# Kernel tuning notes

Measured on AMD Instinct MI355X. Metric: run time of the kernel, lower is better.

## Reference

```python
import jax, jax.numpy as jnp
import numpy as np

N_NODES = 100000
N_EDGES = 3200000
F_IN, H_ENC, H_GCN, H_Q, A_DIM = 128, 128, 128, 256, 10


def setup_inputs() -> dict:
    key = jax.random.key(0)
    ks = jax.random.split(key, 8)
    s = lambda d: 1.0 / np.sqrt(d)
    return {
        "x": jax.random.normal(ks[0], (N_NODES, F_IN), jnp.float32),
        "edge_index": jax.random.randint(ks[1], (2, N_EDGES), 0, N_NODES, jnp.int64),
        "W_enc": jax.random.normal(ks[2], (F_IN, H_ENC), jnp.float32) * s(F_IN),
        "b_enc": jnp.zeros((H_ENC,), jnp.float32),
        "W_gcn": jax.random.normal(ks[3], (H_ENC, H_GCN), jnp.float32) * s(H_ENC),
        "b_gcn": jnp.zeros((H_GCN,), jnp.float32),
        "W1": jax.random.normal(ks[4], (H_GCN, H_Q), jnp.float32) * s(H_GCN),
        "b1": jnp.zeros((H_Q,), jnp.float32),
        "W2": jax.random.normal(ks[5], (H_Q, A_DIM), jnp.float32) * s(H_Q),
        "b2": jnp.zeros((A_DIM,), jnp.float32),
    }


def gcn_conv(x, edge_index, W, b):
    # Standard GCNConv: D^{-1/2} (A + I) D^{-1/2} X W + b, symmetric norm with self-loops.
    n = x.shape[0]
    src, dst = edge_index[0], edge_index[1]
    xw = x @ W  # [N, H]
    deg = jnp.ones((n,), xw.dtype).at[dst].add(1.0)  # in-degree + self-loop
    dinv = jax.lax.rsqrt(deg)
    coef = dinv[src] * dinv[dst]  # [E]
    msg = xw[src] * coef[:, None]  # [E, H] gather-scale
    agg = jax.ops.segment_sum(msg, dst, num_segments=n)  # scatter-add
    agg = agg + xw * (dinv * dinv)[:, None]  # self-loop contribution
    return agg + b


def reference(x, edge_index, W_enc, b_enc, W_gcn, b_gcn, W1, b1, W2, b2):
    h = jax.nn.relu(x @ W_enc + b_enc)              # Encoder: Linear + ReLU
    h = jax.nn.relu(gcn_conv(h, edge_index, W_gcn, b_gcn))  # GCNConv + ReLU
    q = jax.nn.relu(h @ W1 + b1) @ W2 + b2          # Q_Net MLP
    return q
```

## Files before the change

### kernel.cpp

```cpp
#include <hip/hip_runtime.h>

#define N_NODES 100000
constexpr int F     = 128;
constexpr int NB    = (N_NODES + 63) / 64;
constexpr int BCAP  = 2560;
constexpr int LCAP  = 80;
constexpr int CHUNK = 8192;
constexpr int PADN  = N_NODES;

typedef __attribute__((ext_vector_type(8))) short short8;
typedef __attribute__((ext_vector_type(4))) float f32x4;
typedef __attribute__((ext_vector_type(4))) short short4v;
typedef __attribute__((ext_vector_type(4))) unsigned uint4v;

__device__ inline short f2bf(float v) {
    union { float f; unsigned u; } x; x.f = v;
    unsigned r = (x.u + 0x7fff + ((x.u >> 16) & 1)) >> 16;
    return (short)r;
}
__device__ inline float lo_bf(unsigned v) {
    union { unsigned u; float f; } x; x.u = v << 16; return x.f;
}
__device__ inline float hi_bf(unsigned v) {
    union { unsigned u; float f; } x; x.u = v & 0xffff0000u; return x.f;
}

__global__ __launch_bounds__(256) void prep_kernel(const float* __restrict__ W_enc,
                                                   const float* __restrict__ W_gcn,
                                                   const float* __restrict__ W1,
                                                   const float* __restrict__ W2,
                                                   short* __restrict__ Wte,
                                                   short* __restrict__ Wtg,
                                                   short* __restrict__ Wt1,
                                                   short* __restrict__ W2t,
                                                   int* __restrict__ bcr) {
    int idx = blockIdx.x * 256 + threadIdx.x;
    if (idx < 16384) { int h = idx >> 7, k = idx & 127; Wte[idx] = f2bf(W_enc[k * 128 + h]); return; }
    idx -= 16384;
    if (idx < 16384) { int h = idx >> 7, k = idx & 127; Wtg[idx] = f2bf(W_gcn[k * 128 + h]); return; }
    idx -= 16384;
    if (idx < 32768) { int h = idx >> 7, k = idx & 127; Wt1[idx] = f2bf(W1[k * 256 + h]); return; }
    idx -= 32768;
    if (idx < 4096)  { int n = idx >> 8, k = idx & 255; W2t[idx] = (n < 10) ? f2bf(W2[k * 10 + n]) : (short)0; return; }
    idx -= 4096;
    if (idx < NB) bcr[idx] = 0;
}

__global__ __launch_bounds__(512) void part_kernel(const int* __restrict__ src,
                                                   const int* __restrict__ dst,
                                                   int* __restrict__ bcur,
                                                   int* __restrict__ part, int E) {
    __shared__ int cnt[NB];
    __shared__ int base[NB];
    for (int b = threadIdx.x; b < NB; b += 512) cnt[b] = 0;
    __syncthreads();
    const int e0 = blockIdx.x * CHUNK;
    const int e1 = min(e0 + CHUNK, E);
#pragma unroll 4
    for (int e = e0 + threadIdx.x; e < e1; e += 512)
        atomicAdd(&cnt[dst[e] >> 6], 1);
    __syncthreads();
    for (int b = threadIdx.x; b < NB; b += 512) {
        int c = cnt[b];
        base[b] = c ? atomicAdd(&bcur[b], c) : 0;
        cnt[b] = 0;
    }
    __syncthreads();
#pragma unroll 4
    for (int e = e0 + threadIdx.x; e < e1; e += 512) {
        int d = dst[e];
        int b = d >> 6;
        int idx = base[b] + atomicAdd(&cnt[b], 1);
        if (idx < BCAP) part[b * BCAP + idx] = src[e] | ((d & 63) << 17);
    }
}

__global__ __launch_bounds__(256) void gemmA_kernel(const float* __restrict__ x,
                                                    const short* __restrict__ Wte,
                                                    const short* __restrict__ Wtg,
                                                    const float* __restrict__ b_enc,
                                                    const int* __restrict__ bcur,
                                                    const int* __restrict__ part,
                                                    short* __restrict__ xs) {
    __shared__ int deg_l[64];
    __shared__ short h_l[4][16][136];
    const int b = blockIdx.x;
    if (threadIdx.x < 64) deg_l[threadIdx.x] = 0;
    __syncthreads();
    const int cnt = min(bcur[b], BCAP);
    const int* p = part + (size_t)b * BCAP;
#pragma unroll 4
    for (int i = threadIdx.x; i < cnt; i += 256)
        atomicAdd(&deg_l[(p[i] >> 17) & 63], 1);

    const int wave = threadIdx.x >> 6;
    const int lane = threadIdx.x & 63;
    const int quad = lane >> 4;
    const int l16  = lane & 15;
    const int node0 = b * 64 + wave * 16;
    int nrow = node0 + l16;
    const bool valid = nrow < N_NODES;
    if (!valid) nrow = N_NODES - 1;

    f32x4 acc[8] = {};
#pragma unroll
    for (int kc = 0; kc < 4; ++kc) {
        const float* ap = x + (size_t)nrow * 128 + kc * 32 + quad * 8;
        float4 f0 = *reinterpret_cast<const float4*>(ap);
        float4 f1 = *reinterpret_cast<const float4*>(ap + 4);
        short8 xfrag;
        xfrag.s0 = f2bf(f0.x); xfrag.s1 = f2bf(f0.y); xfrag.s2 = f2bf(f0.z); xfrag.s3 = f2bf(f0.w);
        xfrag.s4 = f2bf(f1.x); xfrag.s5 = f2bf(f1.y); xfrag.s6 = f2bf(f1.z); xfrag.s7 = f2bf(f1.w);
#pragma unroll
        for (int t = 0; t < 8; ++t) {
            short8 wfrag = *reinterpret_cast<const short8*>(Wte + (size_t)(t * 16 + l16) * 128 + kc * 32 + quad * 8);
            acc[t] = __builtin_amdgcn_mfma_f32_16x16x32_bf16(wfrag, xfrag, acc[t], 0, 0, 0);
        }
    }
#pragma unroll
    for (int t = 0; t < 8; ++t) {
        short4v o;
#pragma unroll
        for (int r = 0; r < 4; ++r)
            ((short*)&o)[r] = f2bf(fmaxf(acc[t][r] + b_enc[t * 16 + quad * 4 + r], 0.f));
        *reinterpret_cast<short4v*>(&h_l[wave][l16][t * 16 + quad * 4]) = o;
    }
    __syncthreads();

    const float dvn = rsqrtf(1.f + (float)deg_l[wave * 16 + l16]);
    f32x4 acc2[8] = {};
#pragma unroll
    for (int kc = 0; kc < 4; ++kc) {
        short8 xfrag = *reinterpret_cast<const short8*>(&h_l[wave][l16][kc * 32 + quad * 8]);
#pragma unroll
        for (int t = 0; t < 8; ++t) {
            short8 wfrag = *reinterpret_cast<const short8*>(Wtg + (size_t)(t * 16 + l16) * 128 + kc * 32 + quad * 8);
            acc2[t] = __builtin_amdgcn_mfma_f32_16x16x32_bf16(wfrag, xfrag, acc2[t], 0, 0, 0);
        }
    }
    const int srow = node0 + l16;
#pragma unroll
    for (int t = 0; t < 8; ++t) {
        short4v o;
#pragma unroll
        for (int r = 0; r < 4; ++r)
            ((short*)&o)[r] = valid ? f2bf(acc2[t][r] * dvn) : (short)0;
        *reinterpret_cast<short4v*>(xs + (size_t)srow * 128 + t * 16 + quad * 4) = o;
    }
}

__global__ __launch_bounds__(256, 3) void aggB_kernel(const short* __restrict__ xs,
                                                      const int* __restrict__ bcur,
                                                      const int* __restrict__ part,
                                                      const float* __restrict__ bg,
                                                      const short* __restrict__ Wt1,
                                                      const short* __restrict__ W2t,
                                                      const float* __restrict__ b1,
                                                      const float* __restrict__ b2,
                                                      float* __restrict__ q) {
    __shared__ char smemA[64 * LCAP * 4 > 4 * 16 * 264 * 2 ? 64 * LCAP * 4 : 4 * 16 * 264 * 2 + 256];
    __shared__ short h2_l[4][16][136];
    int* csr_l = (int*)smemA;
    int* cur   = (int*)(smemA + 64 * LCAP * 4);

    const int b = blockIdx.x;
    const int tid = threadIdx.x;
    if (tid < 64) cur[tid] = 0;
    __syncthreads();
    const int cnt = min(bcur[b], BCAP);
    const int* p = part + (size_t)b * BCAP;
#pragma unroll 4
    for (int i = tid; i < cnt; i += 256) {
        int v = p[i];
        int ld = (v >> 17) & 63;
        int pos = atomicAdd(&cur[ld], 1);
        if (pos < LCAP) csr_l[ld * LCAP + pos] = v & 0x1FFFF;
    }
    __syncthreads();
    if (tid < 64) {
        int d = min(cur[tid], LCAP);
        int dp = (d + 7) & ~7;
        for (int k = d; k < dp; ++k) csr_l[tid * LCAP + k] = PADN;
    }
    __syncthreads();

    const int wave = tid >> 6;
    const int lane = tid & 63;
    const int g    = lane >> 4;
    const int l16  = lane & 15;
    const uint4v* xs4 = reinterpret_cast<const uint4v*>(xs);
    const float4 bgA = reinterpret_cast<const float4*>(bg)[l16 * 2];
    const float4 bgB = reinterpret_cast<const float4*>(bg)[l16 * 2 + 1];

    for (int t = 0; t < 16; ++t) {
        const int ld = wave * 16 + t;
        const int node = b * 64 + ld;
        if (node >= N_NODES) break;

        const int dtrue = cur[ld];
        const int dpad = (min(dtrue, LCAP) + 7) & ~7;
        const float dv = rsqrtf(1.f + (float)dtrue);
        const int* cl = csr_l + ld * LCAP;

        float a0 = 0.f, a1 = 0.f, a2 = 0.f, a3 = 0.f, a4 = 0.f, a5 = 0.f, a6 = 0.f, a7 = 0.f;
        for (int j = 0; j < dpad; j += 8) {
#pragma unroll
            for (int u = 0; u < 2; ++u) {
                int sj = cl[j + u * 4 + g];
                uint4v v = xs4[((size_t)sj << 4) + l16];
                a0 += lo_bf(v.x); a1 += hi_bf(v.x);
                a2 += lo_bf(v.y); a3 += hi_bf(v.y);
                a4 += lo_bf(v.z); a5 += hi_bf(v.z);
                a6 += lo_bf(v.w); a7 += hi_bf(v.w);
            }
        }
        a0 += __shfl_xor(a0, 16, 64); a0 += __shfl_xor(a0, 32, 64);
        a1 += __shfl_xor(a1, 16, 64); a1 += __shfl_xor(a1, 32, 64);
        a2 += __shfl_xor(a2, 16, 64); a2 += __shfl_xor(a2, 32, 64);
        a3 += __shfl_xor(a3, 16, 64); a3 += __shfl_xor(a3, 32, 64);
        a4 += __shfl_xor(a4, 16, 64); a4 += __shfl_xor(a4, 32, 64);
        a5 += __shfl_xor(a5, 16, 64); a5 += __shfl_xor(a5, 32, 64);
        a6 += __shfl_xor(a6, 16, 64); a6 += __shfl_xor(a6, 32, 64);
        a7 += __shfl_xor(a7, 16, 64); a7 += __shfl_xor(a7, 32, 64);
        if (g == 0) {
            uint4v vs = xs4[((size_t)node << 4) + l16];
            a0 += lo_bf(vs.x); a1 += hi_bf(vs.x);
            a2 += lo_bf(vs.y); a3 += hi_bf(vs.y);
            a4 += lo_bf(vs.z); a5 += hi_bf(vs.z);
            a6 += lo_bf(vs.w); a7 += hi_bf(vs.w);
            short8 o;
            o.s0 = f2bf(fmaxf(fmaf(a0, dv, bgA.x), 0.f));
            o.s1 = f2bf(fmaxf(fmaf(a1, dv, bgA.y), 0.f));
            o.s2 = f2bf(fmaxf(fmaf(a2, dv, bgA.z), 0.f));
            o.s3 = f2bf(fmaxf(fmaf(a3, dv, bgA.w), 0.f));
            o.s4 = f2bf(fmaxf(fmaf(a4, dv, bgB.x), 0.f));
            o.s5 = f2bf(fmaxf(fmaf(a5, dv, bgB.y), 0.f));
            o.s6 = f2bf(fmaxf(fmaf(a6, dv, bgB.z), 0.f));
            o.s7 = f2bf(fmaxf(fmaf(a7, dv, bgB.w), 0.f));
            *reinterpret_cast<short8*>(&h2_l[wave][ld - wave * 16][l16 * 8]) = o;
        }
    }
    __syncthreads();
    short* hq_l = (short*)smemA;

    const int quad = lane >> 4;
    const int node0 = b * 64 + wave * 16;

    f32x4 acc[16] = {};
#pragma unroll
    for (int kc = 0; kc < 4; ++kc) {
        short8 xfrag = *reinterpret_cast<const short8*>(&h2_l[wave][l16][kc * 32 + quad * 8]);
#pragma unroll
        for (int t = 0; t < 16; ++t) {
            short8 wfrag = *reinterpret_cast<const short8*>(Wt1 + (size_t)(t * 16 + l16) * 128 + kc * 32 + quad * 8);
            acc[t] = __builtin_amdgcn_mfma_f32_16x16x32_bf16(wfrag, xfrag, acc[t], 0, 0, 0);
        }
    }
#pragma unroll
    for (int t = 0; t < 16; ++t) {
        short4v o;
#pragma unroll
        for (int r = 0; r < 4; ++r)
            ((short*)&o)[r] = f2bf(fmaxf(acc[t][r] + b1[t * 16 + quad * 4 + r], 0.f));
        *reinterpret_cast<short4v*>(&hq_l[(wave * 16 + l16) * 264 + t * 16 + quad * 4]) = o;
    }

    f32x4 a2 = {};
#pragma unroll
    for (int kc = 0; kc < 8; ++kc) {
        short8 afrag = *reinterpret_cast<const short8*>(&hq_l[(wave * 16 + l16) * 264 + kc * 32 + quad * 8]);
        short8 bfrag = *reinterpret_cast<const short8*>(W2t + (size_t)l16 * 256 + kc * 32 + quad * 8);
        a2 = __builtin_amdgcn_mfma_f32_16x16x32_bf16(afrag, bfrag, a2, 0, 0, 0);
    }
    if (l16 < 10) {
        float bv = b2[l16];
#pragma unroll
        for (int r = 0; r < 4; ++r) {
            int nd = node0 + quad * 4 + r;
            if (nd < N_NODES) q[(size_t)nd * 10 + l16] = a2[r] + bv;
        }
    }
}

extern "C" void kernel_launch(void* const* d_in, const int* in_sizes, int n_in,
                              void* d_out, int out_size, void* d_ws, size_t ws_size,
                              hipStream_t stream) {
    const float* x     = (const float*)d_in[0];
    const int*   ei    = (const int*)d_in[1];
    const float* W_enc = (const float*)d_in[2];
    const float* b_enc = (const float*)d_in[3];
    const float* W_gcn = (const float*)d_in[4];
    const float* b_gcn = (const float*)d_in[5];
    const float* W1    = (const float*)d_in[6];
    const float* b1    = (const float*)d_in[7];
    const float* W2    = (const float*)d_in[8];
    const float* b2    = (const float*)d_in[9];
    float* q = (float*)d_out;

    const int E = in_sizes[1] / 2;
    const int* srcv = ei;
    const int* dstv = ei + E;

    char* ws = (char*)d_ws;
    const size_t XSB = (size_t)(NB * 64) * 128 * sizeof(short);
    short* xs  = (short*)(ws);
    int*   part= (int*)  (ws + XSB);
    char*  tail = ws + XSB + (size_t)NB * BCAP * sizeof(int);
    int*   bcr = (int*)(tail);
    short* Wte = (short*)(tail + 8192);
    short* Wtg = (short*)(tail + 8192 + 32768);
    short* Wt1 = (short*)(tail + 8192 + 65536);
    short* W2t = (short*)(tail + 8192 + 131072);

    prep_kernel<<<279, 256, 0, stream>>>(W_enc, W_gcn, W1, W2, Wte, Wtg, Wt1, W2t, bcr);
    part_kernel<<<(E + CHUNK - 1) / CHUNK, 512, 0, stream>>>(srcv, dstv, bcr, part, E);
    gemmA_kernel<<<NB, 256, 0, stream>>>(x, Wte, Wtg, b_enc, bcr, part, xs);
    aggB_kernel<<<NB, 256, 0, stream>>>(xs, bcr, part, b_gcn, Wt1, W2t, b1, b2, q);
}
```

Before: 402.3 us.

## Split aggregation from Q-MLP GEMM into separate kernels to raise gather occupancy

The fused aggregate-plus-MLP kernel is split in two. A lightweight agg_kernel with 512 threads and high occupancy performs the neighbour gather and writes h2 to global memory. A separate gemmB_kernel then runs the two MFMA layers. The gather loop now issues four independent loads per iteration with padding to 16, exposing more memory-level parallelism. The cost is an extra kernel launch and a global round-trip of the bf16 h2 array (about 25MB).

Measured after the change: 397.9 us. Within noise of the previous version (-1.1%).

```diff
diff --git a/kernel.cpp b/kernel.cpp
--- a/kernel.cpp
+++ b/kernel.cpp
@@ -149,20 +149,13 @@
     }
 }
 
-__global__ __launch_bounds__(256, 3) void aggB_kernel(const short* __restrict__ xs,
-                                                      const int* __restrict__ bcur,
-                                                      const int* __restrict__ part,
-                                                      const float* __restrict__ bg,
-                                                      const short* __restrict__ Wt1,
-                                                      const short* __restrict__ W2t,
-                                                      const float* __restrict__ b1,
-                                                      const float* __restrict__ b2,
-                                                      float* __restrict__ q) {
-    __shared__ char smemA[64 * LCAP * 4 > 4 * 16 * 264 * 2 ? 64 * LCAP * 4 : 4 * 16 * 264 * 2 + 256];
-    __shared__ short h2_l[4][16][136];
-    int* csr_l = (int*)smemA;
-    int* cur   = (int*)(smemA + 64 * LCAP * 4);
-
+__global__ __launch_bounds__(512, 8) void agg_kernel(const short* __restrict__ xs,
+                                                     const int* __restrict__ bcur,
+                                                     const int* __restrict__ part,
+                                                     const float* __restrict__ bg,
+                                                     short* __restrict__ h2) {
+    __shared__ int csr_l[64 * LCAP];
+    __shared__ int cur[64];
     const int b = blockIdx.x;
     const int tid = threadIdx.x;
     if (tid < 64) cur[tid] = 0;
@@ -170,7 +163,7 @@
     const int cnt = min(bcur[b], BCAP);
     const int* p = part + (size_t)b * BCAP;
 #pragma unroll 4
-    for (int i = tid; i < cnt; i += 256) {
+    for (int i = tid; i < cnt; i += 512) {
         int v = p[i];
         int ld = (v >> 17) & 63;
         int pos = atomicAdd(&cur[ld], 1);
@@ -179,7 +172,7 @@
     __syncthreads();
     if (tid < 64) {
         int d = min(cur[tid], LCAP);
-        int dp = (d + 7) & ~7;
+        int dp = (d + 15) & ~15;
         for (int k = d; k < dp; ++k) csr_l[tid * LCAP + k] = PADN;
     }
     __syncthreads();
@@ -192,26 +185,30 @@
     const float4 bgA = reinterpret_cast<const float4*>(bg)[l16 * 2];
     const float4 bgB = reinterpret_cast<const float4*>(bg)[l16 * 2 + 1];
 
-    for (int t = 0; t < 16; ++t) {
-        const int ld = wave * 16 + t;
+    for (int t = 0; t < 8; ++t) {
+        const int ld = wave * 8 + t;
         const int node = b * 64 + ld;
         if (node >= N_NODES) break;
 
         const int dtrue = cur[ld];
-        const int dpad = (min(dtrue, LCAP) + 7) & ~7;
+        const int dpad = (min(dtrue, LCAP) + 15) & ~15;
         const float dv = rsqrtf(1.f + (float)dtrue);
         const int* cl = csr_l + ld * LCAP;
 
         float a0 = 0.f, a1 = 0.f, a2 = 0.f, a3 = 0.f, a4 = 0.f, a5 = 0.f, a6 = 0.f, a7 = 0.f;
-        for (int j = 0; j < dpad; j += 8) {
-#pragma unroll
-            for (int u = 0; u < 2; ++u) {
-                int sj = cl[j + u * 4 + g];
-                uint4v v = xs4[((size_t)sj << 4) + l16];
-                a0 += lo_bf(v.x); a1 += hi_bf(v.x);
-                a2 += lo_bf(v.y); a3 += hi_bf(v.y);
-                a4 += lo_bf(v.z); a5 += hi_bf(v.z);
-                a6 += lo_bf(v.w); a7 += hi_bf(v.w);
+        for (int j = 0; j < dpad; j += 16) {
+            int s[4];
+            uint4v v[4];
+#pragma unroll
+            for (int u = 0; u < 4; ++u) s[u] = cl[j + u * 4 + g];
+#pragma unroll
+            for (int u = 0; u < 4; ++u) v[u] = xs4[((size_t)s[u] << 4) + l16];
+#pragma unroll
+            for (int u = 0; u < 4; ++u) {
+                a0 += lo_bf(v[u].x); a1 += hi_bf(v[u].x);
+                a2 += lo_bf(v[u].y); a3 += hi_bf(v[u].y);
+                a4 += lo_bf(v[u].z); a5 += hi_bf(v[u].z);
+                a6 += lo_bf(v[u].w); a7 += hi_bf(v[u].w);
             }
         }
         a0 += __shfl_xor(a0, 16, 64); a0 += __shfl_xor(a0, 32, 64);
@@ -237,19 +234,30 @@
             o.s5 = f2bf(fmaxf(fmaf(a5, dv, bgB.y), 0.f));
             o.s6 = f2bf(fmaxf(fmaf(a6, dv, bgB.z), 0.f));
             o.s7 = f2bf(fmaxf(fmaf(a7, dv, bgB.w), 0.f));
-            *reinterpret_cast<short8*>(&h2_l[wave][ld - wave * 16][l16 * 8]) = o;
-        }
-    }
-    __syncthreads();
-    short* hq_l = (short*)smemA;
-
+            *reinterpret_cast<short8*>(h2 + ((size_t)node << 7) + l16 * 8) = o;
+        }
+    }
+}
+
+__global__ __launch_bounds__(256) void gemmB_kernel(const short* __restrict__ h2,
+                                                    const short* __restrict__ Wt1,
+                                                    const short* __restrict__ W2t,
+                                                    const float* __restrict__ b1,
+                                                    const float* __restrict__ b2,
+                                                    float* __restrict__ q) {
+    __shared__ short hq_l[4][16][264];
+    const int wave = threadIdx.x >> 6;
+    const int lane = threadIdx.x & 63;
     const int quad = lane >> 4;
-    const int node0 = b * 64 + wave * 16;
+    const int l16  = lane & 15;
+    const int node0 = blockIdx.x * 64 + wave * 16;
+    int nrow = node0 + l16;
+    if (nrow >= N_NODES) nrow = N_NODES - 1;
 
     f32x4 acc[16] = {};
 #pragma unroll
     for (int kc = 0; kc < 4; ++kc) {
-        short8 xfrag = *reinterpret_cast<const short8*>(&h2_l[wave][l16][kc * 32 + quad * 8]);
+        short8 xfrag = *reinterpret_cast<const short8*>(h2 + (size_t)nrow * 128 + kc * 32 + quad * 8);
 #pragma unroll
         for (int t = 0; t < 16; ++t) {
             short8 wfrag = *reinterpret_cast<const short8*>(Wt1 + (size_t)(t * 16 + l16) * 128 + kc * 32 + quad * 8);
@@ -262,13 +270,13 @@
 #pragma unroll
         for (int r = 0; r < 4; ++r)
             ((short*)&o)[r] = f2bf(fmaxf(acc[t][r] + b1[t * 16 + quad * 4 + r], 0.f));
-        *reinterpret_cast<short4v*>(&hq_l[(wave * 16 + l16) * 264 + t * 16 + quad * 4]) = o;
+        *reinterpret_cast<short4v*>(&hq_l[wave][l16][t * 16 + quad * 4]) = o;
     }
 
     f32x4 a2 = {};
 #pragma unroll
     for (int kc = 0; kc < 8; ++kc) {
-        short8 afrag = *reinterpret_cast<const short8*>(&hq_l[(wave * 16 + l16) * 264 + kc * 32 + quad * 8]);
+        short8 afrag = *reinterpret_cast<const short8*>(&hq_l[wave][l16][kc * 32 + quad * 8]);
         short8 bfrag = *reinterpret_cast<const short8*>(W2t + (size_t)l16 * 256 + kc * 32 + quad * 8);
         a2 = __builtin_amdgcn_mfma_f32_16x16x32_bf16(afrag, bfrag, a2, 0, 0, 0);
     }
@@ -304,8 +312,9 @@
     char* ws = (char*)d_ws;
     const size_t XSB = (size_t)(NB * 64) * 128 * sizeof(short);
     short* xs  = (short*)(ws);
-    int*   part= (int*)  (ws + XSB);
-    char*  tail = ws + XSB + (size_t)NB * BCAP * sizeof(int);
+    short* h2  = (short*)(ws + XSB);
+    int*   part= (int*)  (ws + 2 * XSB);
+    char*  tail = ws + 2 * XSB + (size_t)NB * BCAP * sizeof(int);
     int*   bcr = (int*)(tail);
     short* Wte = (short*)(tail + 8192);
     short* Wtg = (short*)(tail + 8192 + 32768);
@@ -315,5 +324,6 @@
     prep_kernel<<<279, 256, 0, stream>>>(W_enc, W_gcn, W1, W2, Wte, Wtg, Wt1, W2t, bcr);
     part_kernel<<<(E + CHUNK - 1) / CHUNK, 512, 0, stream>>>(srcv, dstv, bcr, part, E);
     gemmA_kernel<<<NB, 256, 0, stream>>>(x, Wte, Wtg, b_enc, bcr, part, xs);
-    aggB_kernel<<<NB, 256, 0, stream>>>(xs, bcr, part, b_gcn, Wt1, W2t, b1, b2, q);
-}
+    agg_kernel<<<NB, 512, 0, stream>>>(xs, bcr, part, b_gcn, h2);
+    gemmB_kernel<<<NB, 256, 0, stream>>>(h2, Wt1, W2t, b1, b2, q);
+}
```
